# Optimization experiments

Hardware: AMD Instinct MI355X
Metric: run time of the kernel (lower is better)

Reference implementation:

```python
import jax, jax.numpy as jnp
import numpy as np

D_MODEL = 512
N_HEADS = 8
DEPTH = D_MODEL // N_HEADS
NEG_INF = -1000000000.0


def setup_inputs() -> dict:
    key = jax.random.key(0)
    ks = jax.random.split(key, 12)
    B, S = 4, 2048
    scale = 0.02
    return {
        "Q": jax.random.normal(ks[0], (B, S, D_MODEL), jnp.float32),
        "K": jax.random.normal(ks[1], (B, S, D_MODEL), jnp.float32),
        "V": jax.random.normal(ks[2], (B, S, D_MODEL), jnp.float32),
        "mask": jax.random.randint(ks[3], (B, S, S), 0, 2, jnp.int32),
        "Wq": jax.random.normal(ks[4], (D_MODEL, D_MODEL), jnp.float32) * scale,
        "bq": jnp.zeros((D_MODEL,), jnp.float32),
        "Wk": jax.random.normal(ks[5], (D_MODEL, D_MODEL), jnp.float32) * scale,
        "bk": jnp.zeros((D_MODEL,), jnp.float32),
        "Wv": jax.random.normal(ks[6], (D_MODEL, D_MODEL), jnp.float32) * scale,
        "bv": jnp.zeros((D_MODEL,), jnp.float32),
        "Wo": jax.random.normal(ks[7], (D_MODEL, D_MODEL), jnp.float32) * scale,
        "bo": jnp.zeros((D_MODEL,), jnp.float32),
    }


def _split_heads(x, B):
    # [B, S, d_model] -> [B, H, S, depth]
    S = x.shape[1]
    return x.reshape(B, S, N_HEADS, DEPTH).transpose(0, 2, 1, 3)


def reference(Q, K, V, mask, Wq, bq, Wk, bk, Wv, bv, Wo, bo):
    B, S, _ = Q.shape
    q = _split_heads(Q @ Wq + bq, B)  # [B,H,S,d]
    k = _split_heads(K @ Wk + bk, B)
    v = _split_heads(V @ Wv + bv, B)
    scores = jnp.einsum("bhqd,bhkd->bhqk", q, k) / jnp.sqrt(
        jnp.asarray(DEPTH, jnp.float32))
    m = mask[:, None, :, :]  # broadcast over heads: [B,1,S,S]
    scores = jnp.where(m == 0, jnp.asarray(NEG_INF, scores.dtype), scores)
    attn = jax.nn.softmax(scores, axis=-1)
    ctx = jnp.einsum("bhqk,bhkd->bhqd", attn, v)
    ctx = ctx.transpose(0, 2, 1, 3).reshape(B, S, D_MODEL)
    return ctx @ Wo + bo
```

## Files before the change

kernel.cpp:

```cpp
#include <hip/hip_runtime.h>
#include <hip/hip_bf16.h>
#include <stdint.h>

typedef unsigned short u16;
typedef unsigned int u32;
typedef unsigned long long u64;
using bf16x8 = __attribute__((ext_vector_type(8))) __bf16;
using f32x4  = __attribute__((ext_vector_type(4))) float;
using f32x16 = __attribute__((ext_vector_type(16))) float;

static constexpr int B_ = 4, H_ = 8, S_ = 2048, D_ = 64, DM_ = 512;
#define QSCALE 0.1803368801111601f

__device__ __forceinline__ u16 f2b(float f) {
  u32 u = __float_as_uint(f);
  u = (u + 0x7FFFu + ((u >> 16) & 1u)) >> 16;
  return (u16)u;
}

__device__ __forceinline__ u32 cvtpk_bf16(float a, float b) {
  u32 r;
  asm("v_cvt_pk_bf16_f32 %0, %1, %2" : "=v"(r) : "v"(a), "v"(b));
  return r;
}
__device__ __forceinline__ void plswap(u32& a, u32& b) {
  asm("v_permlane32_swap_b32 %0, %1" : "+v"(a), "+v"(b));
}
__device__ __forceinline__ void gload16(const void* g, void* lds) {
  __builtin_amdgcn_global_load_lds(
      (const __attribute__((address_space(1))) u32*)g,
      (__attribute__((address_space(3))) u32*)lds, 16, 0, 0);
}
#if __has_builtin(__builtin_amdgcn_exp2f)
__device__ __forceinline__ float exp2fast(float x) { return __builtin_amdgcn_exp2f(x); }
#else
__device__ __forceinline__ float exp2fast(float x) {
  float r;
  asm("v_exp_f32 %0, %1" : "=v"(r) : "v"(x));
  return r;
}
#endif
__device__ __forceinline__ float selmask(float ex, u64 pred) {
  float r;
  asm("v_cndmask_b32 %0, 0, %1, %2" : "=v"(r) : "v"(ex), "s"(pred));
  return r;
}

__global__ __launch_bounds__(256) void prep_w_kernel(
    const float* __restrict__ Wq, const float* __restrict__ Wk,
    const float* __restrict__ Wv, const float* __restrict__ Wo,
    u16* __restrict__ Wtq, u16* __restrict__ Wtk, u16* __restrict__ Wtv, u16* __restrict__ Wto) {
  __shared__ float tile[32][33];
  const int z = blockIdx.z;
  const float* W = z == 0 ? Wq : z == 1 ? Wk : z == 2 ? Wv : Wo;
  u16* Wt       = z == 0 ? Wtq : z == 1 ? Wtk : z == 2 ? Wtv : Wto;
  const int k0 = blockIdx.x * 32, n0 = blockIdx.y * 32;
  const int t = threadIdx.x;
  {
    const int kl = t >> 3, nl4 = (t & 7) * 4;
    float4 v = *(const float4*)(W + (size_t)(k0 + kl) * DM_ + n0 + nl4);
    tile[kl][nl4 + 0] = v.x; tile[kl][nl4 + 1] = v.y;
    tile[kl][nl4 + 2] = v.z; tile[kl][nl4 + 3] = v.w;
  }
  __syncthreads();
  {
    const int nl = t >> 3, kl4 = (t & 7) * 4;
    ushort4 o;
    o.x = f2b(tile[kl4 + 0][nl]); o.y = f2b(tile[kl4 + 1][nl]);
    o.z = f2b(tile[kl4 + 2][nl]); o.w = f2b(tile[kl4 + 3][nl]);
    *(ushort4*)(Wt + (size_t)(n0 + nl) * DM_ + k0 + kl4) = o;
  }
}

__global__ __launch_bounds__(256) void pack_mask_kernel(const int* __restrict__ mask,
                                                        u64* __restrict__ wmask) {
  __shared__ int mt[4][32][65];
  const int t = threadIdx.x, lane = t & 63, w = t >> 6;
  const int kt = blockIdx.x * 4 + w, qg = blockIdx.y, b = blockIdx.z;
  const int q0 = qg * 32;
  const int* src = mask + ((size_t)b * S_ + q0) * S_ + kt * 64 + lane;
#pragma unroll 8
  for (int i = 0; i < 32; ++i) mt[w][i][lane] = src[(size_t)i * S_];
  u64* dst = wmask + (((size_t)(b * 64 + qg) * 32 + kt) * 32);
  const int hi4 = (lane >> 5) * 4;
#pragma unroll
  for (int idx = 0; idx < 32; ++idx) {
    const int ksub = idx >> 4, r = idx & 15;
    const int key = ksub * 32 + (r & 3) + 8 * (r >> 2) + hi4;
    u64 bal = __ballot(mt[w][lane & 31][key] != 0);
    if (lane == 0) dst[idx] = bal;
  }
}

__global__ __launch_bounds__(256) void gemm_qkv_kernel(
    const float* __restrict__ Qf, const float* __restrict__ Kf, const float* __restrict__ Vf,
    const u16* __restrict__ Wtq, const u16* __restrict__ Wtk, const u16* __restrict__ Wtv,
    const float* __restrict__ bq, const float* __restrict__ bk, const float* __restrict__ bv,
    u16* __restrict__ qp, u16* __restrict__ kp, u16* __restrict__ vp) {
  __shared__ __align__(16) float As[2][128 * 32];
  __shared__ __align__(16) u16  Bs[2][128 * 32];
  const int z = blockIdx.z;
  const float* A    = z == 0 ? Qf : z == 1 ? Kf : Vf;
  const u16* Bt     = z == 0 ? Wtq : z == 1 ? Wtk : Wtv;
  const float* bias = z == 0 ? bq : z == 1 ? bk : bv;
  u16* outp         = z == 0 ? qp : z == 1 ? kp : vp;
  const float scale = z == 0 ? QSCALE : 1.0f;

  const int t = threadIdx.x;
  const int lane = t & 63, wid = t >> 6;
  const int wr = wid >> 1, wc = wid & 1;
  const int l15 = lane & 15, l4 = lane >> 4;
  const int cn = blockIdx.x * 128, rm = blockIdx.y * 128;

  const int arow = t >> 3, acol = (t & 7) * 4;
  const float* asrc = A + (size_t)(rm + arow) * DM_ + acol;
  const int brow = t >> 2, bcol = (t & 3) * 8;
  const u16* bsrc = Bt + (size_t)(cn + brow) * DM_ + bcol;

  auto stage = [&](int bufi, int k0) {
    char* adst = (char*)As[bufi] + wid * 1024;
    char* bdst = (char*)Bs[bufi] + wid * 1024;
#pragma unroll
    for (int i = 0; i < 4; ++i)
      gload16(asrc + (size_t)(i * 32) * DM_ + k0, adst + i * 4096);
    gload16(bsrc + k0, bdst);
    gload16(bsrc + (size_t)64 * DM_ + k0, bdst + 4096);
  };

  f32x4 acc[4][4] = {};

  stage(0, 0);
  __syncthreads();
  int buf = 0;

  for (int k0 = 0; k0 < DM_; k0 += 32) {
    if (k0 + 32 < DM_) stage(buf ^ 1, k0 + 32);
    bf16x8 af[4], bfr[4];
#pragma unroll
    for (int m = 0; m < 4; ++m) {
      const float* ap = As[buf] + (wr * 64 + m * 16 + l15) * 32 + l4 * 8;
      float4 x = *(const float4*)ap, y = *(const float4*)(ap + 4);
      union { u32 wds[4]; bf16x8 v; } c;
      c.wds[0] = cvtpk_bf16(x.x, x.y); c.wds[1] = cvtpk_bf16(x.z, x.w);
      c.wds[2] = cvtpk_bf16(y.x, y.y); c.wds[3] = cvtpk_bf16(y.z, y.w);
      af[m] = c.v;
    }
#pragma unroll
    for (int n = 0; n < 4; ++n)
      bfr[n] = *(const bf16x8*)((const char*)Bs[buf] + (wc * 64 + n * 16 + l15) * 64 + l4 * 16);
#pragma unroll
    for (int m = 0; m < 4; ++m)
#pragma unroll
      for (int n = 0; n < 4; ++n)
        acc[m][n] = __builtin_amdgcn_mfma_f32_16x16x32_bf16(af[m], bfr[n], acc[m][n], 0, 0, 0);
    __syncthreads();
    buf ^= 1;
  }

#pragma unroll
  for (int m = 0; m < 4; ++m)
#pragma unroll
    for (int n = 0; n < 4; ++n) {
      int col = cn + wc * 64 + n * 16 + l15;
      float bv_ = bias[col];
#pragma unroll
      for (int r = 0; r < 4; ++r) {
        int row = rm + wr * 64 + m * 16 + l4 * 4 + r;
        float v = (acc[m][n][r] + bv_) * scale;
        int b = row >> 11, s = row & 2047;
        int h = col >> 6, d = col & 63;
        if (z < 2)
          outp[(((size_t)(b * H_ + h)) * S_ + s) * D_ + d] = f2b(v);
        else
          outp[(((size_t)(b * H_ + h)) * D_ + d) * S_ + s] = f2b(v);
      }
    }
}

__global__ __launch_bounds__(256) void gemm_out_kernel(
    const u16* __restrict__ A, const u16* __restrict__ Bt,
    const float* __restrict__ bias, float* __restrict__ outp) {
  __shared__ __align__(16) u16 As[2][64 * 32];
  __shared__ __align__(16) u16 Bs[2][128 * 32];
  const int t = threadIdx.x;
  const int lane = t & 63, w = t >> 6;
  const int l15 = lane & 15, l4 = lane >> 4;
  const int cn = blockIdx.x * 128, rm = blockIdx.y * 64;

  const int srow = w * 16 + (lane >> 2), scol = (lane & 3) * 8;
  const u16* asrc = A + (size_t)(rm + srow) * DM_ + scol;
  const u16* bsrc = Bt + (size_t)(cn + srow) * DM_ + scol;

  auto stage = [&](int bufi, int k0) {
    gload16(asrc + k0, (char*)As[bufi] + w * 1024);
    gload16(bsrc + k0, (char*)Bs[bufi] + w * 1024);
    gload16(bsrc + (size_t)64 * DM_ + k0, (char*)Bs[bufi] + w * 1024 + 4096);
  };

  f32x4 acc[4][2] = {};

  stage(0, 0);
  __syncthreads();
  int buf = 0;

  for (int k0 = 0; k0 < DM_; k0 += 32) {
    if (k0 + 32 < DM_) stage(buf ^ 1, k0 + 32);
    bf16x8 af[4], bfr[2];
#pragma unroll
    for (int m = 0; m < 4; ++m)
      af[m] = *(const bf16x8*)((const char*)As[buf] + (m * 16 + l15) * 64 + l4 * 16);
#pragma unroll
    for (int n = 0; n < 2; ++n)
      bfr[n] = *(const bf16x8*)((const char*)Bs[buf] + (w * 32 + n * 16 + l15) * 64 + l4 * 16);
#pragma unroll
    for (int m = 0; m < 4; ++m)
#pragma unroll
      for (int n = 0; n < 2; ++n)
        acc[m][n] = __builtin_amdgcn_mfma_f32_16x16x32_bf16(af[m], bfr[n], acc[m][n], 0, 0, 0);
    __syncthreads();
    buf ^= 1;
  }

#pragma unroll
  for (int m = 0; m < 4; ++m)
#pragma unroll
    for (int n = 0; n < 2; ++n) {
      int col = cn + w * 32 + n * 16 + l15;
      float bv_ = bias[col];
#pragma unroll
      for (int r = 0; r < 4; ++r) {
        int row = rm + m * 16 + l4 * 4 + r;
        outp[(size_t)row * DM_ + col] = acc[m][n][r] + bv_;
      }
    }
}

__global__ __launch_bounds__(256, 4) void attn_kernel(
    const u16* __restrict__ qp, const u16* __restrict__ kp, const u16* __restrict__ vp,
    const u64* __restrict__ wmask, u16* __restrict__ ctx) {
  __shared__ __align__(16) char smem[32768];
  const int t = threadIdx.x, lane = t & 63, w = t >> 6;
  const int l31 = lane & 31, hi = lane >> 5;
  const int ksub = w & 1, qsub = w >> 1;
  const int wu = __builtin_amdgcn_readfirstlane(w);
  const int wgid = blockIdx.x;
  const int h = wgid & 7, idx = wgid >> 3;
  const int b = idx >> 5, qt = idx & 31;
  const size_t head  = ((size_t)(b * H_ + h)) * S_ * D_;
  const size_t headT = ((size_t)(b * H_ + h)) * D_ * S_;
  const int q0 = qt * 64 + qsub * 32;
  const int q  = q0 + l31;

  bf16x8 qf[4];
  {
    const u16* qrow = qp + head + (size_t)q * D_;
#pragma unroll
    for (int ks = 0; ks < 4; ++ks) qf[ks] = *(const bf16x8*)(qrow + ks * 16 + hi * 8);
  }

  const u64* wm = wmask + (((size_t)(b * 64 + qt * 2 + (wu >> 1)) * 32) * 32) + (wu & 1) * 16;

  const int kxor = (l31 & 7) << 4;
  const int krbase = (ksub * 32 + l31) * 128;
  const int rbase0 = l31 * 128, rbase1 = (32 + l31) * 128;
  int colx[4];
#pragma unroll
  for (int s = 0; s < 4; ++s) colx[s] = ((s * 32 + hi * 16) ^ kxor);
  int vcolx[2];
#pragma unroll
  for (int s = 0; s < 2; ++s) vcolx[s] = ((ksub * 64 + s * 32 + hi * 16) ^ kxor);

  const int srow = lane >> 3;
  const int scol = ((lane & 7) ^ srow) << 3;
  const int c0 = w, c1 = w + 4;
  const u16* ksrc0 = kp + head + (size_t)(c0 * 8 + srow) * D_ + scol;
  const u16* ksrc1 = kp + head + (size_t)(c1 * 8 + srow) * D_ + scol;
  const u16* vsrc0 = vp + headT + (size_t)(c0 * 8 + srow) * S_ + scol;
  const u16* vsrc1 = vp + headT + (size_t)(c1 * 8 + srow) * S_ + scol;

  f32x16 accO0, accO1, lacc, FZ;
#pragma unroll
  for (int i = 0; i < 16; ++i) { accO0[i] = 0.f; accO1[i] = 0.f; lacc[i] = 0.f; FZ[i] = 0.f; }
  union { u32 wds[4]; bf16x8 v; } ones;
#pragma unroll
  for (int i = 0; i < 4; ++i) ones.wds[i] = 0x3F803F80u;

  auto stage = [&](int bufi, int kt) {
    char* kb = smem + bufi * 8192;
    char* vb = smem + 16384 + bufi * 8192;
    gload16(ksrc0 + (size_t)kt * 4096, kb + c0 * 1024);
    gload16(ksrc1 + (size_t)kt * 4096, kb + c1 * 1024);
    gload16(vsrc0 + kt * 64, vb + c0 * 1024);
    gload16(vsrc1 + kt * 64, vb + c1 * 1024);
  };

  stage(0, 0);
  u64 mskr[16];
#pragma unroll
  for (int r = 0; r < 16; ++r) mskr[r] = wm[r];
  __syncthreads();
  int buf = 0;

  for (int kt = 0; kt < S_ / 64; ++kt) {
    if (kt < S_ / 64 - 1) stage(buf ^ 1, kt + 1);

    const char* kb = smem + buf * 8192;
    const char* vb = smem + 16384 + buf * 8192;

    f32x16 s;
    {
      bf16x8 kf[4];
#pragma unroll
      for (int ks = 0; ks < 4; ++ks) kf[ks] = *(const bf16x8*)(kb + krbase + colx[ks]);
      __builtin_amdgcn_s_setprio(1);
      s = __builtin_amdgcn_mfma_f32_32x32x16_bf16(kf[0], qf[0], FZ, 0, 0, 0);
#pragma unroll
      for (int ks = 1; ks < 4; ++ks)
        s = __builtin_amdgcn_mfma_f32_32x32x16_bf16(kf[ks], qf[ks], s, 0, 0, 0);
      __builtin_amdgcn_s_setprio(0);
    }

    float e[16];
#pragma unroll
    for (int r = 0; r < 16; ++r) e[r] = selmask(exp2fast(s[r]), mskr[r]);

    {
      u32 pw[8];
#pragma unroll
      for (int j = 0; j < 8; ++j)
        pw[j] = cvtpk_bf16(e[2 * j], e[2 * j + 1]);
      plswap(pw[0], pw[2]); plswap(pw[1], pw[3]);
      plswap(pw[4], pw[6]); plswap(pw[5], pw[7]);
      __builtin_amdgcn_s_setprio(1);
#pragma unroll
      for (int s2 = 0; s2 < 2; ++s2) {
        union { u32 wds[4]; bf16x8 v; } pa;
        pa.wds[0] = pw[s2 * 4 + 0]; pa.wds[1] = pw[s2 * 4 + 1];
        pa.wds[2] = pw[s2 * 4 + 2]; pa.wds[3] = pw[s2 * 4 + 3];
        bf16x8 vf0 = *(const bf16x8*)(vb + rbase0 + vcolx[s2]);
        accO0 = __builtin_amdgcn_mfma_f32_32x32x16_bf16(pa.v, vf0, accO0, 0, 0, 0);
        bf16x8 vf1 = *(const bf16x8*)(vb + rbase1 + vcolx[s2]);
        accO1 = __builtin_amdgcn_mfma_f32_32x32x16_bf16(pa.v, vf1, accO1, 0, 0, 0);
        lacc = __builtin_amdgcn_mfma_f32_32x32x16_bf16(pa.v, ones.v, lacc, 0, 0, 0);
      }
      __builtin_amdgcn_s_setprio(0);
    }

    if (kt < S_ / 64 - 1) {
      const u64* wmk = wm + (kt + 1) * 32;
#pragma unroll
      for (int r = 0; r < 16; ++r) mskr[r] = wmk[r];
    }
    __syncthreads();
    buf ^= 1;
  }

  float (*Ol)[32][64] = (float (*)[32][64])smem;
  float (*La)[32] = (float (*)[32])(smem + 16384);
  if (ksub == 1) {
#pragma unroll
    for (int r = 0; r < 16; ++r) {
      const int qr = (r & 3) + 8 * (r >> 2) + 4 * hi;
      Ol[qsub][qr][l31]      = accO0[r];
      Ol[qsub][qr][32 + l31] = accO1[r];
      if (l31 == 0) La[qsub][qr] = lacc[r];
    }
  }
  __syncthreads();
  if (ksub == 0) {
    const int colA = h * 64 + l31, colB = h * 64 + 32 + l31;
#pragma unroll
    for (int r = 0; r < 16; ++r) {
      const int qr = (r & 3) + 8 * (r >> 2) + 4 * hi;
      const int row = q0 + qr;
      const float inv = 1.0f / (lacc[r] + La[qsub][qr]);
      u16* o = ctx + ((size_t)(b * S_) + row) * DM_;
      o[colA] = f2b((accO0[r] + Ol[qsub][qr][l31])      * inv);
      o[colB] = f2b((accO1[r] + Ol[qsub][qr][32 + l31]) * inv);
    }
  }
}

extern "C" void kernel_launch(void* const* d_in, const int* in_sizes, int n_in,
                              void* d_out, int out_size, void* d_ws, size_t ws_size,
                              hipStream_t stream) {
  const float* Q  = (const float*)d_in[0];
  const float* K  = (const float*)d_in[1];
  const float* V  = (const float*)d_in[2];
  const int* mask = (const int*)d_in[3];
  const float* Wq = (const float*)d_in[4];
  const float* bq = (const float*)d_in[5];
  const float* Wk = (const float*)d_in[6];
  const float* bk = (const float*)d_in[7];
  const float* Wv = (const float*)d_in[8];
  const float* bv = (const float*)d_in[9];
  const float* Wo = (const float*)d_in[10];
  const float* bo = (const float*)d_in[11];

  char* ws = (char*)d_ws;
  size_t off = 0;
  auto alloc = [&](size_t bytes) -> void* {
    void* p = ws + off;
    off += (bytes + 255) & ~(size_t)255;
    return p;
  };
  const size_t act_b = (size_t)B_ * S_ * DM_ * 2;
  u16* Wtq = (u16*)alloc((size_t)DM_ * DM_ * 2);
  u16* Wtk = (u16*)alloc((size_t)DM_ * DM_ * 2);
  u16* Wtv = (u16*)alloc((size_t)DM_ * DM_ * 2);
  u16* Wto = (u16*)alloc((size_t)DM_ * DM_ * 2);
  u64* wmask = (u64*)alloc((size_t)B_ * 64 * 32 * 32 * 8);
  u16* qp  = (u16*)alloc(act_b);
  u16* kp  = (u16*)alloc(act_b);
  u16* vp  = (u16*)alloc(act_b);
  u16* ctx = (u16*)alloc(act_b);

  prep_w_kernel<<<dim3(16, 16, 4), 256, 0, stream>>>(Wq, Wk, Wv, Wo, Wtq, Wtk, Wtv, Wto);
  pack_mask_kernel<<<dim3(8, 64, 4), 256, 0, stream>>>(mask, wmask);

  gemm_qkv_kernel<<<dim3(4, 64, 3), 256, 0, stream>>>(
      Q, K, V, Wtq, Wtk, Wtv, bq, bk, bv, qp, kp, vp);

  attn_kernel<<<dim3(1024), 256, 0, stream>>>(qp, kp, vp, wmask, ctx);

  gemm_out_kernel<<<dim3(4, 128), 256, 0, stream>>>(ctx, Wto, bo, (float*)d_out);
}
```

Baseline: 130.3 us.

## Fuse mask packing into QKV GEMM kernel with interleaved block roles

```diff
diff --git a/kernel.cpp b/kernel.cpp
--- a/kernel.cpp
+++ b/kernel.cpp
@@ -72,45 +72,49 @@
   }
 }
 
-__global__ __launch_bounds__(256) void pack_mask_kernel(const int* __restrict__ mask,
-                                                        u64* __restrict__ wmask) {
-  __shared__ int mt[4][32][65];
-  const int t = threadIdx.x, lane = t & 63, w = t >> 6;
-  const int kt = blockIdx.x * 4 + w, qg = blockIdx.y, b = blockIdx.z;
-  const int q0 = qg * 32;
-  const int* src = mask + ((size_t)b * S_ + q0) * S_ + kt * 64 + lane;
-#pragma unroll 8
-  for (int i = 0; i < 32; ++i) mt[w][i][lane] = src[(size_t)i * S_];
-  u64* dst = wmask + (((size_t)(b * 64 + qg) * 32 + kt) * 32);
-  const int hi4 = (lane >> 5) * 4;
-#pragma unroll
-  for (int idx = 0; idx < 32; ++idx) {
-    const int ksub = idx >> 4, r = idx & 15;
-    const int key = ksub * 32 + (r & 3) + 8 * (r >> 2) + hi4;
-    u64 bal = __ballot(mt[w][lane & 31][key] != 0);
-    if (lane == 0) dst[idx] = bal;
-  }
-}
-
-__global__ __launch_bounds__(256) void gemm_qkv_kernel(
+__global__ __launch_bounds__(256) void qkv_pack_kernel(
     const float* __restrict__ Qf, const float* __restrict__ Kf, const float* __restrict__ Vf,
     const u16* __restrict__ Wtq, const u16* __restrict__ Wtk, const u16* __restrict__ Wtv,
     const float* __restrict__ bq, const float* __restrict__ bk, const float* __restrict__ bv,
-    u16* __restrict__ qp, u16* __restrict__ kp, u16* __restrict__ vp) {
-  __shared__ __align__(16) float As[2][128 * 32];
-  __shared__ __align__(16) u16  Bs[2][128 * 32];
-  const int z = blockIdx.z;
+    u16* __restrict__ qp, u16* __restrict__ kp, u16* __restrict__ vp,
+    const int* __restrict__ mask, u64* __restrict__ wmask) {
+  __shared__ __align__(16) char smem[49152];
+  const int g = blockIdx.x;
+  const int sel = g % 11, base = g / 11;
+  const int t = threadIdx.x;
+  const int lane = t & 63, wid = t >> 6;
+
+  if (sel >= 3) {
+    const int p = base * 8 + (sel - 3);
+    const int x = p & 7, y = (p >> 3) & 63, zb = p >> 9;
+    const int kt = x * 4 + wid, qg = y, b = zb;
+    int* mt = (int*)(smem + wid * 8320);
+    const int* src = mask + ((size_t)b * S_ + qg * 32) * S_ + kt * 64 + lane;
+#pragma unroll 8
+    for (int j = 0; j < 32; ++j) mt[j * 65 + lane] = src[(size_t)j * S_];
+    u64* dst = wmask + (((size_t)(b * 64 + qg) * 32 + kt) * 32);
+    const int hi4 = (lane >> 5) * 4;
+#pragma unroll
+    for (int idx = 0; idx < 32; ++idx) {
+      const int ksub = idx >> 4, r = idx & 15;
+      const int key = ksub * 32 + (r & 3) + 8 * (r >> 2) + hi4;
+      u64 bal = __ballot(mt[(lane & 31) * 65 + key] != 0);
+      if (lane == 0) dst[idx] = bal;
+    }
+    return;
+  }
+
+  const int q = base * 3 + sel;
+  const int z = q >> 8, rem = q & 255;
   const float* A    = z == 0 ? Qf : z == 1 ? Kf : Vf;
   const u16* Bt     = z == 0 ? Wtq : z == 1 ? Wtk : Wtv;
   const float* bias = z == 0 ? bq : z == 1 ? bk : bv;
   u16* outp         = z == 0 ? qp : z == 1 ? kp : vp;
   const float scale = z == 0 ? QSCALE : 1.0f;
 
-  const int t = threadIdx.x;
-  const int lane = t & 63, wid = t >> 6;
   const int wr = wid >> 1, wc = wid & 1;
   const int l15 = lane & 15, l4 = lane >> 4;
-  const int cn = blockIdx.x * 128, rm = blockIdx.y * 128;
+  const int cn = (rem & 3) * 128, rm = (rem >> 2) * 128;
 
   const int arow = t >> 3, acol = (t & 7) * 4;
   const float* asrc = A + (size_t)(rm + arow) * DM_ + acol;
@@ -118,8 +122,8 @@
   const u16* bsrc = Bt + (size_t)(cn + brow) * DM_ + bcol;
 
   auto stage = [&](int bufi, int k0) {
-    char* adst = (char*)As[bufi] + wid * 1024;
-    char* bdst = (char*)Bs[bufi] + wid * 1024;
+    char* adst = smem + bufi * 16384 + wid * 1024;
+    char* bdst = smem + 32768 + bufi * 8192 + wid * 1024;
 #pragma unroll
     for (int i = 0; i < 4; ++i)
       gload16(asrc + (size_t)(i * 32) * DM_ + k0, adst + i * 4096);
@@ -135,10 +139,12 @@
 
   for (int k0 = 0; k0 < DM_; k0 += 32) {
     if (k0 + 32 < DM_) stage(buf ^ 1, k0 + 32);
+    const float* Ab = (const float*)(smem + buf * 16384);
+    const char*  Bb = smem + 32768 + buf * 8192;
     bf16x8 af[4], bfr[4];
 #pragma unroll
     for (int m = 0; m < 4; ++m) {
-      const float* ap = As[buf] + (wr * 64 + m * 16 + l15) * 32 + l4 * 8;
+      const float* ap = Ab + (wr * 64 + m * 16 + l15) * 32 + l4 * 8;
       float4 x = *(const float4*)ap, y = *(const float4*)(ap + 4);
       union { u32 wds[4]; bf16x8 v; } c;
       c.wds[0] = cvtpk_bf16(x.x, x.y); c.wds[1] = cvtpk_bf16(x.z, x.w);
@@ -147,7 +153,7 @@
     }
 #pragma unroll
     for (int n = 0; n < 4; ++n)
-      bfr[n] = *(const bf16x8*)((const char*)Bs[buf] + (wc * 64 + n * 16 + l15) * 64 + l4 * 16);
+      bfr[n] = *(const bf16x8*)(Bb + (wc * 64 + n * 16 + l15) * 64 + l4 * 16);
 #pragma unroll
     for (int m = 0; m < 4; ++m)
 #pragma unroll
@@ -416,10 +422,9 @@
   u16* ctx = (u16*)alloc(act_b);
 
   prep_w_kernel<<<dim3(16, 16, 4), 256, 0, stream>>>(Wq, Wk, Wv, Wo, Wtq, Wtk, Wtv, Wto);
-  pack_mask_kernel<<<dim3(8, 64, 4), 256, 0, stream>>>(mask, wmask);
-
-  gemm_qkv_kernel<<<dim3(4, 64, 3), 256, 0, stream>>>(
-      Q, K, V, Wtq, Wtk, Wtv, bq, bk, bv, qp, kp, vp);
+
+  qkv_pack_kernel<<<dim3(2816), 256, 0, stream>>>(
+      Q, K, V, Wtq, Wtk, Wtv, bq, bk, bv, qp, kp, vp, mask, wmask);
 
   attn_kernel<<<dim3(1024), 256, 0, stream>>>(qp, kp, vp, wmask, ctx);
 
```

Measured after the change: 149.8 us. 15.0% more time.

## Restructure QKV GEMM with register staging, bf16 LDS tiles, and XCD-aware block mapping

Applied to the files above, without the earlier changes.

```diff
diff --git a/kernel.cpp b/kernel.cpp
--- a/kernel.cpp
+++ b/kernel.cpp
@@ -44,6 +44,11 @@
   float r;
   asm("v_cndmask_b32 %0, 0, %1, %2" : "=v"(r) : "v"(ex), "s"(pred));
   return r;
+}
+__device__ __forceinline__ void lgkm_barrier() {
+  asm volatile("s_waitcnt lgkmcnt(0)" ::: "memory");
+  __builtin_amdgcn_s_barrier();
+  __builtin_amdgcn_sched_barrier(0);
 }
 
 __global__ __launch_bounds__(256) void prep_w_kernel(
@@ -97,76 +102,90 @@
     const u16* __restrict__ Wtq, const u16* __restrict__ Wtk, const u16* __restrict__ Wtv,
     const float* __restrict__ bq, const float* __restrict__ bk, const float* __restrict__ bv,
     u16* __restrict__ qp, u16* __restrict__ kp, u16* __restrict__ vp) {
-  __shared__ __align__(16) float As[2][128 * 32];
-  __shared__ __align__(16) u16  Bs[2][128 * 32];
-  const int z = blockIdx.z;
+  __shared__ __align__(16) u16 As[128 * 36];
+  __shared__ __align__(16) u16 Bs[64 * 36];
+  const int g = blockIdx.x;
+  const int x = g & 7, local = g >> 3;
+  const int pair = x * 24 + (local >> 3), n = local & 7;
+  const int z = pair >> 6, m = pair & 63;
   const float* A    = z == 0 ? Qf : z == 1 ? Kf : Vf;
   const u16* Bt     = z == 0 ? Wtq : z == 1 ? Wtk : Wtv;
   const float* bias = z == 0 ? bq : z == 1 ? bk : bv;
   u16* outp         = z == 0 ? qp : z == 1 ? kp : vp;
   const float scale = z == 0 ? QSCALE : 1.0f;
+  const int cn = n * 64, rm = m * 128;
 
   const int t = threadIdx.x;
   const int lane = t & 63, wid = t >> 6;
   const int wr = wid >> 1, wc = wid & 1;
   const int l15 = lane & 15, l4 = lane >> 4;
-  const int cn = blockIdx.x * 128, rm = blockIdx.y * 128;
-
-  const int arow = t >> 3, acol = (t & 7) * 4;
-  const float* asrc = A + (size_t)(rm + arow) * DM_ + acol;
-  const int brow = t >> 2, bcol = (t & 3) * 8;
-  const u16* bsrc = Bt + (size_t)(cn + brow) * DM_ + bcol;
-
-  auto stage = [&](int bufi, int k0) {
-    char* adst = (char*)As[bufi] + wid * 1024;
-    char* bdst = (char*)Bs[bufi] + wid * 1024;
-#pragma unroll
-    for (int i = 0; i < 4; ++i)
-      gload16(asrc + (size_t)(i * 32) * DM_ + k0, adst + i * 4096);
-    gload16(bsrc + k0, bdst);
-    gload16(bsrc + (size_t)64 * DM_ + k0, bdst + 4096);
+
+  const int arow = t >> 1, ah = t & 1;
+  const float* asrc0 = A + (size_t)(rm + arow) * DM_ + ah * 16;
+  char* adst = (char*)As + arow * 72 + ah * 32;
+  const int brow = t >> 2, bqt = t & 3;
+  const u16* bsrc0 = Bt + (size_t)(cn + brow) * DM_ + bqt * 8;
+  char* bdst = (char*)Bs + brow * 72 + bqt * 16;
+
+  float4 ra0, ra1, ra2, ra3;
+  uint4 rb;
+  auto load_regs = [&](int k0) {
+    const float* ap = asrc0 + k0;
+    ra0 = *(const float4*)(ap + 0);
+    ra1 = *(const float4*)(ap + 4);
+    ra2 = *(const float4*)(ap + 8);
+    ra3 = *(const float4*)(ap + 12);
+    rb = *(const uint4*)(bsrc0 + k0);
   };
-
-  f32x4 acc[4][4] = {};
-
-  stage(0, 0);
-  __syncthreads();
-  int buf = 0;
+  auto cvt_write = [&]() {
+    uint4 w0, w1;
+    w0.x = cvtpk_bf16(ra0.x, ra0.y); w0.y = cvtpk_bf16(ra0.z, ra0.w);
+    w0.z = cvtpk_bf16(ra1.x, ra1.y); w0.w = cvtpk_bf16(ra1.z, ra1.w);
+    w1.x = cvtpk_bf16(ra2.x, ra2.y); w1.y = cvtpk_bf16(ra2.z, ra2.w);
+    w1.z = cvtpk_bf16(ra3.x, ra3.y); w1.w = cvtpk_bf16(ra3.z, ra3.w);
+    *(uint4*)(adst)      = w0;
+    *(uint4*)(adst + 16) = w1;
+    *(uint4*)(bdst)      = rb;
+  };
+
+  f32x4 acc[4][2] = {};
+
+  load_regs(0);
+  cvt_write();
+  lgkm_barrier();
 
   for (int k0 = 0; k0 < DM_; k0 += 32) {
-    if (k0 + 32 < DM_) stage(buf ^ 1, k0 + 32);
-    bf16x8 af[4], bfr[4];
-#pragma unroll
-    for (int m = 0; m < 4; ++m) {
-      const float* ap = As[buf] + (wr * 64 + m * 16 + l15) * 32 + l4 * 8;
-      float4 x = *(const float4*)ap, y = *(const float4*)(ap + 4);
-      union { u32 wds[4]; bf16x8 v; } c;
-      c.wds[0] = cvtpk_bf16(x.x, x.y); c.wds[1] = cvtpk_bf16(x.z, x.w);
-      c.wds[2] = cvtpk_bf16(y.x, y.y); c.wds[3] = cvtpk_bf16(y.z, y.w);
-      af[m] = c.v;
-    }
-#pragma unroll
-    for (int n = 0; n < 4; ++n)
-      bfr[n] = *(const bf16x8*)((const char*)Bs[buf] + (wc * 64 + n * 16 + l15) * 64 + l4 * 16);
-#pragma unroll
-    for (int m = 0; m < 4; ++m)
-#pragma unroll
-      for (int n = 0; n < 4; ++n)
-        acc[m][n] = __builtin_amdgcn_mfma_f32_16x16x32_bf16(af[m], bfr[n], acc[m][n], 0, 0, 0);
-    __syncthreads();
-    buf ^= 1;
-  }
-
-#pragma unroll
-  for (int m = 0; m < 4; ++m)
-#pragma unroll
-    for (int n = 0; n < 4; ++n) {
-      int col = cn + wc * 64 + n * 16 + l15;
+    const bool more = (k0 + 32 < DM_);
+    if (more) load_regs(k0 + 32);
+    bf16x8 af[4], bfr[2];
+#pragma unroll
+    for (int mm = 0; mm < 4; ++mm)
+      af[mm] = *(const bf16x8*)((const char*)As + (wr * 64 + mm * 16 + l15) * 72 + l4 * 16);
+#pragma unroll
+    for (int nn = 0; nn < 2; ++nn)
+      bfr[nn] = *(const bf16x8*)((const char*)Bs + (wc * 32 + nn * 16 + l15) * 72 + l4 * 16);
+#pragma unroll
+    for (int mm = 0; mm < 4; ++mm)
+#pragma unroll
+      for (int nn = 0; nn < 2; ++nn)
+        acc[mm][nn] = __builtin_amdgcn_mfma_f32_16x16x32_bf16(af[mm], bfr[nn], acc[mm][nn], 0, 0, 0);
+    if (more) {
+      lgkm_barrier();
+      cvt_write();
+      lgkm_barrier();
+    }
+  }
+
+#pragma unroll
+  for (int mm = 0; mm < 4; ++mm)
+#pragma unroll
+    for (int nn = 0; nn < 2; ++nn) {
+      int col = cn + wc * 32 + nn * 16 + l15;
       float bv_ = bias[col];
 #pragma unroll
       for (int r = 0; r < 4; ++r) {
-        int row = rm + wr * 64 + m * 16 + l4 * 4 + r;
-        float v = (acc[m][n][r] + bv_) * scale;
+        int row = rm + wr * 64 + mm * 16 + l4 * 4 + r;
+        float v = (acc[mm][nn][r] + bv_) * scale;
         int b = row >> 11, s = row & 2047;
         int h = col >> 6, d = col & 63;
         if (z < 2)
@@ -418,7 +437,7 @@
   prep_w_kernel<<<dim3(16, 16, 4), 256, 0, stream>>>(Wq, Wk, Wv, Wo, Wtq, Wtk, Wtv, Wto);
   pack_mask_kernel<<<dim3(8, 64, 4), 256, 0, stream>>>(mask, wmask);
 
-  gemm_qkv_kernel<<<dim3(4, 64, 3), 256, 0, stream>>>(
+  gemm_qkv_kernel<<<dim3(1536), 256, 0, stream>>>(
       Q, K, V, Wtq, Wtk, Wtv, bq, bk, bv, qp, kp, vp);
 
   attn_kernel<<<dim3(1024), 256, 0, stream>>>(qp, kp, vp, wmask, ctx);
```

Result: slower. 154.0 us (+18.2%).
